# Performance work log

Hardware: AMD Instinct MI355X
Metric: run time of the kernel (lower is better)

The kernel has to match this reference:

```python
import jax, jax.numpy as jnp
import numpy as np

B, NK = 32, 1024
NUM_SAMPLES = 512
IT_MATCHES = 4
IT_RANSAC = 8
NUM_CORR = 5
INLIER_3D_TH = 0.15
INLIER_REF_TH = 0.15
NUM_REF_STEPS = 4
SCORE_TEMP = 10.0
TH_OUTLIERS = 0.35
MAX_LOSS_NULL = 0.5
SOFT_CLIP_M = 0.5
BETA = 5.0 / INLIER_3D_TH


def _gumbel(key, shape):
    u = jax.random.uniform(key, shape, minval=1e-6, maxval=1.0 - 1e-6)
    return -jnp.log(-jnp.log(u))


def _backproject(cor, d, K):
    # cor [B,S,2], d [B,S,2] (channel 0 is depth), K [B,3,3] -> [B,S,3]
    depth = d[..., :1]
    pts = jnp.concatenate([cor, jnp.ones_like(cor[..., :1])], -1)
    Kinv = jnp.linalg.inv(K)
    rays = jnp.einsum('bij,bsj->bsi', Kinv, pts)
    return depth * rays


def _procrustes(X, Y, w):
    # weighted Kabsch: find R,t with Y ~ R X + t. X,Y [B,N,3], w [B,N]
    wn = w / (jnp.sum(w, -1, keepdims=True) + 1e-8)
    muX = jnp.einsum('bn,bni->bi', wn, X)
    muY = jnp.einsum('bn,bni->bi', wn, Y)
    Xc = X - muX[:, None]
    Yc = Y - muY[:, None]
    H = jnp.einsum('bn,bni,bnj->bij', wn, Xc, Yc)  # [B,3,3]
    U, S, Vt = jnp.linalg.svd(H, full_matrices=False)
    V = jnp.swapaxes(Vt, -1, -2)
    Ut = jnp.swapaxes(U, -1, -2)
    d = jnp.linalg.det(V @ Ut)
    Vm = V * jnp.stack([jnp.ones_like(d), jnp.ones_like(d), d], -1)[:, None, :]
    R = Vm @ Ut
    t = muY - jnp.einsum('bij,bj->bi', R, muX)
    return R, t[:, None, :]


def _dist(X, Y, R, t):
    return jnp.linalg.norm(jnp.einsum('bij,bnj->bni', R, X) + t - Y, axis=-1)


def _pose_loss(R, t, Rgt, tgt):
    cosang = jnp.clip((jnp.einsum('bij,bij->b', R, Rgt) - 1.0) / 2.0, -0.999999, 0.999999)
    ang = jnp.arccos(cosang)
    terr = jnp.linalg.norm(t - tgt, axis=-1)[:, 0]
    sc = lambda x: SOFT_CLIP_M * jnp.tanh(x / SOFT_CLIP_M)
    lr = sc(ang)[:, None]
    lt = sc(terr)[:, None]
    return 0.5 * (lr + lt), lr, lt


def _rodrigues(axis, ang):
    x, y, z = axis[:, 0], axis[:, 1], axis[:, 2]
    zero = jnp.zeros_like(x)
    Kx = jnp.stack([zero, -z, y, z, zero, -x, -y, x, zero], -1).reshape(-1, 3, 3)
    I = jnp.eye(3, dtype=axis.dtype)[None]
    return I + jnp.sin(ang)[:, None, None] * Kx + (1.0 - jnp.cos(ang))[:, None, None] * (Kx @ Kx)


def setup_inputs():
    ks = jax.random.split(jax.random.key(0), 10)
    matches = jax.random.uniform(ks[0], (B, NK, NK), jnp.float32, 1e-4, 1.0)
    kps0 = jax.random.uniform(ks[1], (B, 2, NK), jnp.float32, 0.0, 640.0)
    kps1 = jax.random.uniform(ks[2], (B, 2, NK), jnp.float32, 0.0, 640.0)
    depth0 = jax.random.uniform(ks[3], (B, 2, NK), jnp.float32, 0.1, 10.0)
    depth1 = jax.random.uniform(ks[4], (B, 2, NK), jnp.float32, 0.1, 10.0)
    Kc = jnp.tile(jnp.array([[600.0, 0.0, 320.0], [0.0, 600.0, 240.0], [0.0, 0.0, 1.0]], jnp.float32)[None], (B, 1, 1))
    axis = jax.random.normal(ks[5], (B, 3))
    axis = axis / (jnp.linalg.norm(axis, axis=-1, keepdims=True) + 1e-8)
    ang = jax.random.uniform(ks[6], (B,), minval=0.0, maxval=0.5)
    R = _rodrigues(axis, ang)
    tvec = 0.3 * jax.random.normal(ks[7], (B, 3))
    T = jnp.zeros((B, 4, 4), jnp.float32).at[:, :3, :3].set(R).at[:, :3, 3].set(tvec).at[:, 3, 3].set(1.0)
    return dict(matches=matches, kps0=kps0, depth0=depth0, kps1=kps1, depth1=depth1,
                K0=Kc, K1=Kc, Kori_color0=Kc, T_0to1=T)


def _forward(matches, kps0, depth0, kps1, depth1, K0, K1, T_0to1):
    Rgt = T_0to1[:, :3, :3]
    tgt = T_0to1[:, :3, 3][:, None, :]
    matches_row = matches.reshape(B, NK * NK)
    logm = jnp.log(matches_row + 1e-12)
    bidx = jnp.arange(B)[:, None]
    kps0t = jnp.swapaxes(kps0, 1, 2)  # [B,NK,2]
    kps1t = jnp.swapaxes(kps1, 1, 2)
    d0t = jnp.swapaxes(depth0, 1, 2)
    d1t = jnp.swapaxes(depth1, 1, 2)
    key = jax.random.key(42)
    total = jnp.zeros((B, 1), jnp.float32)
    for _i in range(IT_MATCHES):
        key, km = jax.random.split(key)
        # multinomial-without-replacement via Gumbel top-k over the full match matrix
        _, sidx = jax.lax.top_k(logm + _gumbel(km, logm.shape), NUM_SAMPLES)  # [B,S]
        i0 = sidx // NK
        i1 = sidx % NK
        cor0 = kps0t[bidx, i0]
        cor1 = kps1t[bidx, i1]
        dd0 = d0t[bidx, i0]
        dd1 = d1t[bidx, i1]
        w = matches_row[bidx, sidx]  # sampling weights for RANSAC minimal sets
        X = _backproject(cor0, dd0, K0)
        Y = _backproject(cor1, dd1, K1)
        logw = jnp.log(w + 1e-12)
        scores, lvals = [], []
        for _kk in range(IT_RANSAC):
            key, kr = jax.random.split(key)
            _, ridx = jax.lax.top_k(logw + _gumbel(kr, logw.shape), NUM_CORR)  # [B,C]
            Xk = X[bidx, ridx]
            Yk = Y[bidx, ridx]
            R_pre, t_pre = _procrustes(Xk, Yk, jnp.ones((B, NUM_CORR), X.dtype))  # use_weights=False
            score_k = jnp.sum(jax.nn.sigmoid(BETA * (INLIER_3D_TH - _dist(X, Y, R_pre, t_pre))), -1, keepdims=True)
            # inlier refinement (no_grad in original)
            Xd = jax.lax.stop_gradient(X)
            Yd = jax.lax.stop_gradient(Y)
            Rd = jax.lax.stop_gradient(R_pre)
            td = jax.lax.stop_gradient(t_pre)
            inl_ref = jnp.zeros((B, NUM_SAMPLES), X.dtype).at[bidx, ridx].set(1.0)
            inl_pre = jnp.zeros((B,), X.dtype)
            for _r in range(NUM_REF_STEPS):
                inl = (_dist(Xd, Yd, Rd, td) < INLIER_REF_TH).astype(X.dtype)
                cnt = inl.sum(-1)
                do = (cnt >= NUM_CORR) & (cnt > inl_pre)
                inl_pre = cnt
                inl_ref = jnp.where(do[:, None], inl, inl_ref)
                Rn, tn = _procrustes(Xd, Yd, inl_ref)
                Rd = jnp.where(do[:, None, None], Rn, Rd)
                td = jnp.where(do[:, None, None], tn, td)
            R, t = _procrustes(X, Y, inl_ref)  # differentiable final fit
            lv, _lr, _lt = _pose_loss(R, t, Rgt, tgt)
            scores.append(score_k)
            lvals.append(lv)
        scores_r = jnp.concatenate(scores, -1)  # [B,IT_RANSAC]
        lvals_r = jnp.concatenate(lvals, -1)
        null_score = TH_OUTLIERS * NUM_SAMPLES * jnp.ones((B, 1), jnp.float32)
        null_loss = MAX_LOSS_NULL * jnp.ones((B, 1), jnp.float32)
        scores_n = jnp.concatenate([scores_r, null_score], -1)
        lvals_n = jnp.concatenate([lvals_r, null_loss], -1)
        sm = jax.nn.softmax(scores_n / SCORE_TEMP, -1)
        total = total + jnp.sum(lvals_n * sm, -1, keepdims=True)
    return total / IT_MATCHES


def reference(matches, kps0, depth0, kps1, depth1, K0, K1, Kori_color0, T_0to1):
    return _forward(matches, kps0, depth0, kps1, depth1, K0, K1, T_0to1)
```

## Files before the change

### kernel.cpp

```cpp
#include <hip/hip_runtime.h>
#include <stdint.h>

typedef unsigned long long u64;
typedef uint32_t u32;

#define NB 32
#define NKP 1024
#define ROWN (NKP*NKP)
#define NSAMP 512
#define ITM 4
#define ITR 8
#define NBIN 2048
#define KBASE 0xC0000000u
#define CHUNKS 64
#define SLOTS 256
#define WQ 352

struct Keys { u32 km[ITM][2]; u32 kr[ITM][ITR][2]; };

__host__ __device__ static inline u32 rotl32(u32 x, int d) { return __builtin_rotateleft32(x, (unsigned)d); }

__host__ __device__ static inline void tf2x32(u32 k0, u32 k1, u32 x0, u32 x1, u32& o0, u32& o1)
{
    u32 ks2 = k0 ^ k1 ^ 0x1BD11BDAu;
    x0 += k0; x1 += k1;
#define TFR(r) { x0 += x1; x1 = rotl32(x1, r); x1 ^= x0; }
    TFR(13) TFR(15) TFR(26) TFR(6)
    x0 += k1; x1 += ks2 + 1u;
    TFR(17) TFR(29) TFR(16) TFR(24)
    x0 += ks2; x1 += k0 + 2u;
    TFR(13) TFR(15) TFR(26) TFR(6)
    x0 += k0; x1 += k1 + 3u;
    TFR(17) TFR(29) TFR(16) TFR(24)
    x0 += k1; x1 += ks2 + 4u;
    TFR(13) TFR(15) TFR(26) TFR(6)
    x0 += ks2; x1 += k0 + 5u;
#undef TFR
    o0 = x0; o1 = x1;
}

__device__ static inline void tf4(const Keys& K, u32 flat, u32 bits[ITM])
{
    u32 x0[ITM], x1[ITM];
    #pragma unroll
    for (int i = 0; i < ITM; ++i) {
        x0[i] = K.km[i][0];
        x1[i] = flat + K.km[i][1];
    }
#define R4(rot) { _Pragma("unroll") \
    for (int i = 0; i < ITM; ++i) { x0[i] += x1[i]; x1[i] = rotl32(x1[i], rot); x1[i] ^= x0[i]; } }
#define INJ(a_expr, b_expr) { _Pragma("unroll") \
    for (int i = 0; i < ITM; ++i) { u32 k0 = K.km[i][0], k1 = K.km[i][1]; \
        u32 ks2 = k0 ^ k1 ^ 0x1BD11BDAu; (void)k0; (void)k1; (void)ks2; \
        x0[i] += (a_expr); x1[i] += (b_expr); } }
    R4(13) R4(15) R4(26) R4(6)
    INJ(k1,      ks2 + 1u)
    R4(17) R4(29) R4(16) R4(24)
    INJ(ks2,     k0 + 2u)
    R4(13) R4(15) R4(26) R4(6)
    INJ(k0,      k1 + 3u)
    R4(17) R4(29) R4(16) R4(24)
    INJ(k1,      ks2 + 4u)
    R4(13) R4(15) R4(26) R4(6)
    INJ(ks2,     k0 + 5u)
#undef R4
#undef INJ
    #pragma unroll
    for (int i = 0; i < ITM; ++i) bits[i] = x0[i] ^ x1[i];
}

#define G_MINV 1e-6f
#define G_MAXV ((float)(1.0 - 1e-6))
#define G_SPAN (G_MAXV - G_MINV)

__device__ static inline float u_from_bits(u32 bits) {
    float f = __uint_as_float((bits >> 9) | 0x3f800000u) - 1.0f;
    float u = __fadd_rn(__fmul_rn(f, G_SPAN), G_MINV);
    return fmaxf(G_MINV, u);
}

#define EARLY_TH9 (8220000u << 9)

__device__ static inline u32 fkey(float v) {
    u32 u = __float_as_uint(v);
    return (u & 0x80000000u) ? ~u : (u | 0x80000000u);
}

__device__ static inline float wred(float v) {
    #pragma unroll
    for (int o = 1; o < 64; o <<= 1) v += __shfl_xor(v, o, 64);
    return v;
}

__device__ static inline u64 shfl_xor_u64(u64 v, int mask) {
    u32 lo = (u32)v, hi = (u32)(v >> 32);
    lo = __shfl_xor(lo, mask, 64);
    hi = __shfl_xor(hi, mask, 64);
    return ((u64)hi << 32) | (u64)lo;
}

__device__ static void kabsch(const float Hf[9], float Rf[9])
{
    double H00=Hf[0],H01=Hf[1],H02=Hf[2];
    double H10=Hf[3],H11=Hf[4],H12=Hf[5];
    double H20=Hf[6],H21=Hf[7],H22=Hf[8];
    double A00 = H00*H00 + H10*H10 + H20*H20;
    double A01 = H00*H01 + H10*H11 + H20*H21;
    double A02 = H00*H02 + H10*H12 + H20*H22;
    double A11 = H01*H01 + H11*H11 + H21*H21;
    double A12 = H01*H02 + H11*H12 + H21*H22;
    double A22 = H02*H02 + H12*H12 + H22*H22;
    double V00=1,V10=0,V20=0;
    double V01=0,V11=1,V21=0;
    double V02=0,V12=0,V22=1;
#define JROT(App,Aqq,Apq,Apr,Aqr, Vp0,Vp1,Vp2, Vq0,Vq1,Vq2) \
    if (fabs(Apq) > 0.0) { \
        double th = (Aqq - App) / (2.0 * Apq); \
        double tt = copysign(1.0, th) / (fabs(th) + sqrt(1.0 + th*th)); \
        double cc = 1.0 / sqrt(1.0 + tt*tt); \
        double ss = tt * cc; \
        double npp = App - tt*Apq, nqq = Aqq + tt*Apq; \
        double npr = cc*Apr - ss*Aqr, nqr = ss*Apr + cc*Aqr; \
        App = npp; Aqq = nqq; Apq = 0.0; Apr = npr; Aqr = nqr; \
        double tv; \
        tv = cc*Vp0 - ss*Vq0; Vq0 = ss*Vp0 + cc*Vq0; Vp0 = tv; \
        tv = cc*Vp1 - ss*Vq1; Vq1 = ss*Vp1 + cc*Vq1; Vp1 = tv; \
        tv = cc*Vp2 - ss*Vq2; Vq2 = ss*Vp2 + cc*Vq2; Vp2 = tv; \
    }
    for (int sw = 0; sw < 5; ++sw) {
        JROT(A00,A11,A01, A02,A12, V00,V10,V20, V01,V11,V21);
        JROT(A00,A22,A02, A01,A12, V00,V10,V20, V02,V12,V22);
        JROT(A11,A22,A12, A01,A02, V01,V11,V21, V02,V12,V22);
    }
#undef JROT
    double l0=A00, l1=A11, l2=A22;
    double e0[3]={V00,V10,V20}, e1[3]={V01,V11,V21}, e2[3]={V02,V12,V22};
    if (l0 < l1) { double t=l0;l0=l1;l1=t; for(int c=0;c<3;++c){double s=e0[c];e0[c]=e1[c];e1[c]=s;} }
    if (l0 < l2) { double t=l0;l0=l2;l2=t; for(int c=0;c<3;++c){double s=e0[c];e0[c]=e2[c];e2[c]=s;} }
    if (l1 < l2) { double t=l1;l1=l2;l2=t; for(int c=0;c<3;++c){double s=e1[c];e1[c]=e2[c];e2[c]=s;} }
    double u0[3], u1[3], u2[3];
#define HMUL(e,u) { u[0]=H00*e[0]+H01*e[1]+H02*e[2]; u[1]=H10*e[0]+H11*e[1]+H12*e[2]; u[2]=H20*e[0]+H21*e[1]+H22*e[2]; }
    HMUL(e0,u0) HMUL(e1,u1) HMUL(e2,u2)
#undef HMUL
    double s0 = sqrt(u0[0]*u0[0]+u0[1]*u0[1]+u0[2]*u0[2]);
    double s1 = sqrt(u1[0]*u1[0]+u1[1]*u1[1]+u1[2]*u1[2]);
    double s2 = sqrt(u2[0]*u2[0]+u2[1]*u2[1]+u2[2]*u2[2]);
    double eps = 1e-12 + 1e-6 * s0;
    if (s0 > 0.0) { u0[0]/=s0; u0[1]/=s0; u0[2]/=s0; } else { u0[0]=1.0; u0[1]=0.0; u0[2]=0.0; }
    if (s1 > eps) { u1[0]/=s1; u1[1]/=s1; u1[2]/=s1; }
    else {
        double ax0 = (fabs(u0[0]) < 0.9) ? 1.0 : 0.0;
        double ax1 = 1.0 - ax0;
        double dd = ax0*u0[0] + ax1*u0[1];
        double w0 = ax0 - dd*u0[0], w1 = ax1 - dd*u0[1], w2 = -dd*u0[2];
        double nn = sqrt(w0*w0+w1*w1+w2*w2);
        u1[0]=w0/nn; u1[1]=w1/nn; u1[2]=w2/nn;
    }
    if (s2 > eps) { u2[0]/=s2; u2[1]/=s2; u2[2]/=s2; }
    else {
        u2[0] = u0[1]*u1[2] - u0[2]*u1[1];
        u2[1] = u0[2]*u1[0] - u0[0]*u1[2];
        u2[2] = u0[0]*u1[1] - u0[1]*u1[0];
    }
    double M[3][3];
    #pragma unroll
    for (int i2=0;i2<3;++i2)
      #pragma unroll
      for (int j2=0;j2<3;++j2)
        M[i2][j2] = e0[i2]*u0[j2] + e1[i2]*u1[j2] + e2[i2]*u2[j2];
    double det = M[0][0]*(M[1][1]*M[2][2]-M[1][2]*M[2][1])
               - M[0][1]*(M[1][0]*M[2][2]-M[1][2]*M[2][0])
               + M[0][2]*(M[1][0]*M[2][1]-M[1][1]*M[2][0]);
    #pragma unroll
    for (int i2=0;i2<3;++i2)
      #pragma unroll
      for (int j2=0;j2<3;++j2)
        Rf[i2*3+j2] = (float)(e0[i2]*u0[j2] + e1[i2]*u1[j2] + det*(e2[i2]*u2[j2]));
}

__device__ static inline float dist1(const float R[9], const float t[3], const float x[3], const float y[3])
{
    float a = R[0]*x[0]+R[1]*x[1]+R[2]*x[2]+t[0]-y[0];
    float b = R[3]*x[0]+R[4]*x[1]+R[5]*x[2]+t[1]-y[1];
    float c = R[6]*x[0]+R[7]*x[1]+R[8]*x[2]+t[2]-y[2];
    return sqrtf(a*a+b*b+c*c);
}

__device__ static void proc512(const float (&X)[8][3], const float (&Y)[8][3], const float (&w)[8],
                               float R[9], float t[3])
{
    float sw = 0.f;
    #pragma unroll
    for (int q=0;q<8;++q) sw += w[q];
    float S = wred(sw) + 1e-8f;
    float wn[8];
    #pragma unroll
    for (int q=0;q<8;++q) wn[q] = w[q] / S;
    float mx[3], my[3];
    #pragma unroll
    for (int c=0;c<3;++c) {
        float ax=0.f, ay=0.f;
        #pragma unroll
        for (int q=0;q<8;++q) { ax += wn[q]*X[q][c]; ay += wn[q]*Y[q][c]; }
        mx[c] = wred(ax); my[c] = wred(ay);
    }
    float Hf[9];
    #pragma unroll
    for (int ci=0;ci<3;++ci)
      #pragma unroll
      for (int cj=0;cj<3;++cj) {
        float h=0.f;
        #pragma unroll
        for (int q=0;q<8;++q) h += wn[q]*(X[q][ci]-mx[ci])*(Y[q][cj]-my[cj]);
        Hf[ci*3+cj] = wred(h);
      }
    kabsch(Hf, R);
    #pragma unroll
    for (int c=0;c<3;++c) t[c] = my[c] - (R[c*3+0]*mx[0] + R[c*3+1]*mx[1] + R[c*3+2]*mx[2]);
}

__device__ static void inv3(const float* __restrict__ Kin, float* __restrict__ out)
{
    float a[3][6];
    for (int r=0;r<3;++r) for (int c=0;c<3;++c) { a[r][c]=Kin[r*3+c]; a[r][c+3] = (r==c)?1.f:0.f; }
    for (int col=0; col<3; ++col) {
        int piv = col;
        for (int r=col+1;r<3;++r) if (fabsf(a[r][col]) > fabsf(a[piv][col])) piv = r;
        if (piv != col) for (int c=0;c<6;++c) { float tt=a[col][c]; a[col][c]=a[piv][c]; a[piv][c]=tt; }
        float pv = a[col][col];
        for (int c=0;c<6;++c) a[col][c] /= pv;
        for (int r=0;r<3;++r) if (r != col) {
            float f = a[r][col];
            if (f != 0.f) for (int c=0;c<6;++c) a[r][c] -= f * a[col][c];
        }
    }
    for (int r=0;r<3;++r) for (int c=0;c<3;++c) out[r*3+c] = a[r][c+3];
}

static const size_t OFF_CNTS = 0;
static const size_t OFF_SC   = OFF_CNTS + (size_t)ITM*NB*CHUNKS*4;
static const size_t OFF_LV   = OFF_SC   + (size_t)ITM*NB*ITR*4;
static const size_t OFF_SAMP = OFF_LV   + (size_t)ITM*NB*ITR*4;
static const size_t OFF_CAND = OFF_SAMP + (size_t)ITM*NB*NSAMP*8*4;

__device__ static inline void drain1(u64 e, float m, u64 (*lists)[SLOTS], u32* lcnt)
{
    u32 bits = (u32)(e >> 32);
    u32 i2 = ((u32)e >> 20) & 3u;
    u32 jj = (u32)e & 0xFFFFFu;
    float u = u_from_bits(bits);
    float g = -logf(-logf(u));
    float v = logf(m + 1e-12f) + g;
    if (v > 4.0f) {
        u32 p = atomicAdd(&lcnt[i2], 1u);
        if (p < (u32)SLOTS) lists[i2][p] = ((u64)fkey(v) << 32) | (u64)(u32)(~jj);
    }
}

__global__ __launch_bounds__(256) void kA(const float* __restrict__ mat, Keys keys,
                                          u64* __restrict__ candC, u32* __restrict__ cnts)
{
    __shared__ u64 lists[ITM][SLOTS];
    __shared__ u32 lcnt[ITM];
    __shared__ u64 q[4][WQ];
    int tid = threadIdx.x;
    int lane = tid & 63;
    int wid = tid >> 6;
    u64 lmask_lt = (1ull << lane) - 1ull;
    if (tid < ITM) lcnt[tid] = 0;
    __syncthreads();
    int b = blockIdx.y;
    int chunk = blockIdx.x;
    const float* rowb = mat + (size_t)b * ROWN;
    u32 jbase = (u32)chunk * 16384u + (u32)tid;
    for (int seg = 0; seg < 2; ++seg) {
        u32 cnt = 0;
        #pragma unroll 1
        for (int lp = 0; lp < 32; ++lp) {
            u32 j = jbase + (u32)((seg*32 + lp) << 8);
            u32 flat = ((u32)b << 20) | j;
            u32 bits[ITM];
            tf4(keys, flat, bits);
            #pragma unroll
            for (int i = 0; i < ITM; ++i) {
                bool hit = (bits[i] >= EARLY_TH9);
                u64 mask = __ballot(hit);
                if (hit) {
                    u32 pos = cnt + (u32)__popcll(mask & lmask_lt);
                    if (pos < (u32)WQ)
                        q[wid][pos] = ((u64)bits[i] << 32) | ((u64)(u32)i << 20) | (u64)j;
                }
                cnt += (u32)__popcll(mask);
            }
        }
        u32 qn = (cnt > (u32)WQ) ? (u32)WQ : cnt;
        for (u32 t0 = (u32)lane; t0 < qn; t0 += 256) {
            u32 t1 = t0 + 64, t2 = t0 + 128, t3 = t0 + 192;
            u64 e0 = q[wid][t0];
            float m0 = rowb[(u32)e0 & 0xFFFFFu];
            u64 e1 = 0, e2 = 0, e3 = 0;
            float m1 = 0.f, m2 = 0.f, m3 = 0.f;
            if (t1 < qn) { e1 = q[wid][t1]; m1 = rowb[(u32)e1 & 0xFFFFFu]; }
            if (t2 < qn) { e2 = q[wid][t2]; m2 = rowb[(u32)e2 & 0xFFFFFu]; }
            if (t3 < qn) { e3 = q[wid][t3]; m3 = rowb[(u32)e3 & 0xFFFFFu]; }
            drain1(e0, m0, lists, lcnt);
            if (t1 < qn) drain1(e1, m1, lists, lcnt);
            if (t2 < qn) drain1(e2, m2, lists, lcnt);
            if (t3 < qn) drain1(e3, m3, lists, lcnt);
        }
    }
    __syncthreads();
    #pragma unroll
    for (int i = 0; i < ITM; ++i) {
        u32 n = lcnt[i]; if (n > (u32)SLOTS) n = SLOTS;
        for (u32 s = tid; s < n; s += 256)
            candC[(((size_t)(i*NB + b))*CHUNKS + chunk)*SLOTS + s] = lists[i][s];
    }
    if (tid < ITM) cnts[((size_t)(tid*NB + b))*CHUNKS + chunk] = min(lcnt[tid], (u32)SLOTS);
}

__global__ __launch_bounds__(512) void kDE(const float* __restrict__ mat,
        const float* __restrict__ kps0, const float* __restrict__ dep0,
        const float* __restrict__ kps1, const float* __restrict__ dep1,
        const float* __restrict__ K0, const float* __restrict__ K1,
        const float* __restrict__ Tmat, Keys keys,
        const u64* __restrict__ candC, const u32* __restrict__ cnts,
        float* __restrict__ scoreArr, float* __restrict__ lvArr)
{
    int ib = blockIdx.x;
    int b = ib % NB;
    int i = ib / NB;
    int tid = threadIdx.x;
    int lane = tid & 63;
    int wid = tid >> 6;
    __shared__ u32 hist[NBIN];
    __shared__ u64 buf[1024];
    __shared__ float sampL[NSAMP][9];
    __shared__ u32 ccnt[CHUNKS];
    __shared__ u32 gs[64];
    __shared__ u32 nkeep, cutkey_s;
    __shared__ float Ki[2][9];
    for (int idx = tid; idx < NBIN; idx += 512) hist[idx] = 0;
    for (int idx = tid; idx < 1024; idx += 512) buf[idx] = 0ull;
    if (tid < CHUNKS) ccnt[tid] = cnts[(size_t)ib*CHUNKS + tid];
    if (tid == 0) nkeep = 0;
    __syncthreads();
    const u64* cd = candC + (size_t)ib * CHUNKS * SLOTS;
    for (int t = tid; t < CHUNKS*SLOTS; t += 512) {
        int c = t >> 8, s = t & (SLOTS-1);
        if ((u32)s < ccnt[c]) {
            u32 key = (u32)(cd[t] >> 32);
            u32 bin = (key - KBASE) >> 14;
            if (bin > (u32)(NBIN-1)) bin = NBIN-1;
            atomicAdd(&hist[bin], 1u);
        }
    }
    __syncthreads();
    if (tid < 64) {
        u32 ssum = 0;
        int top = NBIN-1 - tid*32;
        for (int k = 0; k < 32; ++k) ssum += hist[top - k];
        gs[tid] = ssum;
    }
    __syncthreads();
    if (tid == 0) {
        u32 cum = 0; int cutbin = -1;
        for (int g = 0; g < 64; ++g) {
            if (cum + gs[g] >= (u32)NSAMP) {
                int t2 = NBIN-1 - g*32;
                for (int k = 0; k < 32; ++k) {
                    u32 c = hist[t2 - k];
                    if (cum + c >= (u32)NSAMP) { cutbin = t2 - k; break; }
                    cum += c;
                }
                break;
            }
            cum += gs[g];
        }
        cutkey_s = (cutbin >= 0) ? (KBASE + ((u32)cutbin << 14)) : 0u;
    }
    __syncthreads();
    u32 cutkey = cutkey_s;
    for (int t = tid; t < CHUNKS*SLOTS; t += 512) {
        int c = t >> 8, s = t & (SLOTS-1);
        if ((u32)s < ccnt[c]) {
            u64 cv = cd[t];
            if ((u32)(cv >> 32) >= cutkey) {
                u32 p = atomicAdd(&nkeep, 1u);
                if (p < 1024u) buf[p] = cv;
            }
        }
    }
    __syncthreads();
    for (int k = 2; k <= 1024; k <<= 1) {
        for (int j = k >> 1; j > 0; j >>= 1) {
            for (int i2 = tid; i2 < 1024; i2 += 512) {
                int ixj = i2 ^ j;
                if (ixj > i2) {
                    bool up = ((i2 & k) == 0);
                    u64 a = buf[i2], c2 = buf[ixj];
                    bool dosw = up ? (a > c2) : (a < c2);
                    if (dosw) { buf[i2] = c2; buf[ixj] = a; }
                }
            }
            __syncthreads();
        }
    }
    if (tid == 0) { inv3(K0 + (size_t)b*9, Ki[0]); inv3(K1 + (size_t)b*9, Ki[1]); }
    __syncthreads();
    {
        int r = tid;
        if (r < NSAMP) {
            u64 c = buf[1023 - r];
            u32 j = (~(u32)(c & 0xFFFFFFFFull)) & (u32)(ROWN - 1);
            int i0 = (int)(j >> 10);
            int i1 = (int)(j & 1023u);
            float uu0 = kps0[(size_t)b*2*NKP + i0];
            float vv0 = kps0[(size_t)b*2*NKP + NKP + i0];
            float dd0 = dep0[(size_t)b*2*NKP + i0];
            float uu1 = kps1[(size_t)b*2*NKP + i1];
            float vv1 = kps1[(size_t)b*2*NKP + NKP + i1];
            float dd1 = dep1[(size_t)b*2*NKP + i1];
            float r0 = Ki[0][0]*uu0 + Ki[0][1]*vv0 + Ki[0][2];
            float r1 = Ki[0][3]*uu0 + Ki[0][4]*vv0 + Ki[0][5];
            float r2 = Ki[0][6]*uu0 + Ki[0][7]*vv0 + Ki[0][8];
            float q0 = Ki[1][0]*uu1 + Ki[1][1]*vv1 + Ki[1][2];
            float q1 = Ki[1][3]*uu1 + Ki[1][4]*vv1 + Ki[1][5];
            float q2 = Ki[1][6]*uu1 + Ki[1][7]*vv1 + Ki[1][8];
            float w = mat[(size_t)b*ROWN + j];
            sampL[r][0] = dd0*r0; sampL[r][1] = dd0*r1; sampL[r][2] = dd0*r2;
            sampL[r][3] = dd1*q0; sampL[r][4] = dd1*q1; sampL[r][5] = dd1*q2;
            sampL[r][6] = logf(w + 1e-12f);
        }
    }
    __syncthreads();
    int kk = wid;
    float X[8][3], Y[8][3], lw[8];
    #pragma unroll
    for (int q2 = 0; q2 < 8; ++q2) {
        const float* sp = &sampL[q2*64 + lane][0];
        X[q2][0]=sp[0]; X[q2][1]=sp[1]; X[q2][2]=sp[2];
        Y[q2][0]=sp[3]; Y[q2][1]=sp[4]; Y[q2][2]=sp[5];
        lw[q2]=sp[6];
    }
    u64 comp[8];
    #pragma unroll
    for (int q2 = 0; q2 < 8; ++q2) {
        u32 j = (u32)(q2*64 + lane);
        u32 o0,o1; tf2x32(keys.kr[i][kk][0], keys.kr[i][kk][1], 0u, (u32)(b*NSAMP) + j, o0,o1);
        float u = u_from_bits(o0^o1);
        float g = -logf(-logf(u));
        float v = lw[q2] + g;
        comp[q2] = ((u64)fkey(v) << 32) | (u64)(u32)(~j);
    }
    int ridx[5];
    #pragma unroll
    for (int r = 0; r < 5; ++r) {
        u64 m = comp[0];
        #pragma unroll
        for (int q2=1;q2<8;++q2) if (comp[q2] > m) m = comp[q2];
        #pragma unroll
        for (int o=1;o<64;o<<=1) { u64 x = shfl_xor_u64(m,o); if (x > m) m = x; }
        ridx[r] = (int)((~(u32)(m & 0xFFFFFFFFull)) & (u32)(NSAMP-1));
        #pragma unroll
        for (int q2=0;q2<8;++q2) if (comp[q2] == m) comp[q2] = 0ull;
    }
    float Xk[5][3], Yk[5][3];
    #pragma unroll
    for (int r=0;r<5;++r) {
        const float* p = &sampL[ridx[r]][0];
        Xk[r][0]=p[0]; Xk[r][1]=p[1]; Xk[r][2]=p[2];
        Yk[r][0]=p[3]; Yk[r][1]=p[4]; Yk[r][2]=p[5];
    }
    float S5 = 5.0f + 1e-8f;
    float wn5 = 1.0f / S5;
    float mx[3]={0,0,0}, my[3]={0,0,0};
    #pragma unroll
    for (int r=0;r<5;++r) {
        #pragma unroll
        for (int c=0;c<3;++c) { mx[c] += wn5*Xk[r][c]; my[c] += wn5*Yk[r][c]; }
    }
    float Hf[9] = {0,0,0,0,0,0,0,0,0};
    #pragma unroll
    for (int r=0;r<5;++r)
      #pragma unroll
      for (int ci=0;ci<3;++ci)
        #pragma unroll
        for (int cj=0;cj<3;++cj)
          Hf[ci*3+cj] += wn5*(Xk[r][ci]-mx[ci])*(Yk[r][cj]-my[cj]);
    float Rpre[9], tpre[3];
    kabsch(Hf, Rpre);
    #pragma unroll
    for (int c=0;c<3;++c) tpre[c] = my[c] - (Rpre[c*3+0]*mx[0] + Rpre[c*3+1]*mx[1] + Rpre[c*3+2]*mx[2]);
    const float BETAF = (float)(5.0/0.15);
    float partial = 0.f;
    #pragma unroll
    for (int q2=0;q2<8;++q2) {
        float d = dist1(Rpre, tpre, X[q2], Y[q2]);
        float z = BETAF * (0.15f - d);
        partial += 1.0f / (1.0f + expf(-z));
    }
    float score = wred(partial);
    float inlref[8];
    #pragma unroll
    for (int q2=0;q2<8;++q2) {
        int j = q2*64 + lane;
        inlref[q2] = (j==ridx[0] || j==ridx[1] || j==ridx[2] || j==ridx[3] || j==ridx[4]) ? 1.0f : 0.0f;
    }
    float Rd[9], td[3];
    #pragma unroll
    for (int c2=0;c2<9;++c2) Rd[c2]=Rpre[c2];
    td[0]=tpre[0]; td[1]=tpre[1]; td[2]=tpre[2];
    float inl_pre = 0.f;
    for (int step=0; step<4; ++step) {
        float inl[8]; float csum = 0.f;
        #pragma unroll
        for (int q2=0;q2<8;++q2) {
            float d = dist1(Rd, td, X[q2], Y[q2]);
            inl[q2] = (d < 0.15f) ? 1.0f : 0.0f;
            csum += inl[q2];
        }
        float cnt = wred(csum);
        bool doit = (cnt >= 5.0f) && (cnt > inl_pre);
        inl_pre = cnt;
        if (doit) {
            #pragma unroll
            for (int q2=0;q2<8;++q2) inlref[q2] = inl[q2];
            proc512(X, Y, inlref, Rd, td);
        }
    }
    float Rfin[9], tfin[3];
    proc512(X, Y, inlref, Rfin, tfin);
    const float* Tb = Tmat + (size_t)b*16;
    float tr = 0.f;
    #pragma unroll
    for (int ci=0;ci<3;++ci)
      #pragma unroll
      for (int cj=0;cj<3;++cj)
        tr += Rfin[ci*3+cj] * Tb[ci*4+cj];
    float cosang = (tr - 1.0f) * 0.5f;
    cosang = fminf(fmaxf(cosang, -0.999999f), 0.999999f);
    float ang = acosf(cosang);
    float d0 = tfin[0]-Tb[3], d1 = tfin[1]-Tb[7], d2 = tfin[2]-Tb[11];
    float terr = sqrtf(d0*d0 + d1*d1 + d2*d2);
    float lr = 0.5f * tanhf(ang / 0.5f);
    float lt = 0.5f * tanhf(terr / 0.5f);
    float lv = 0.5f * (lr + lt);
    if (lane == 0) { scoreArr[ib*ITR + kk] = score; lvArr[ib*ITR + kk] = lv; }
}

__global__ void kF(const float* __restrict__ scoreArr, const float* __restrict__ lvArr, float* __restrict__ out)
{
    int b = threadIdx.x;
    if (b >= NB) return;
    const float NULLSC = (float)(0.35 * 512.0);
    float total = 0.f;
    for (int i = 0; i < ITM; ++i) {
        float x[9], lvv[9], ee[9];
        for (int k = 0; k < 8; ++k) {
            x[k] = scoreArr[(i*NB + b)*ITR + k] / 10.0f;
            lvv[k] = lvArr[(i*NB + b)*ITR + k];
        }
        x[8] = NULLSC / 10.0f;
        lvv[8] = 0.5f;
        float m = x[0];
        for (int k = 1; k < 9; ++k) m = fmaxf(m, x[k]);
        float Ssum = 0.f;
        for (int k = 0; k < 9; ++k) { ee[k] = expf(x[k] - m); Ssum += ee[k]; }
        float acc = 0.f;
        for (int k = 0; k < 9; ++k) acc += lvv[k] * (ee[k] / Ssum);
        total += acc;
    }
    out[b] = total / 4.0f;
}

extern "C" void kernel_launch(void* const* d_in, const int* in_sizes, int n_in,
                              void* d_out, int out_size, void* d_ws, size_t ws_size,
                              hipStream_t stream)
{
    (void)in_sizes; (void)n_in; (void)out_size; (void)ws_size;
    const float* mat  = (const float*)d_in[0];
    const float* kps0 = (const float*)d_in[1];
    const float* dep0 = (const float*)d_in[2];
    const float* kps1 = (const float*)d_in[3];
    const float* dep1 = (const float*)d_in[4];
    const float* K0   = (const float*)d_in[5];
    const float* K1   = (const float*)d_in[6];
    const float* Tm   = (const float*)d_in[8];
    float* out = (float*)d_out;

    Keys keys;
    {
        u32 k0 = 0u, k1 = 42u;
        for (int i = 0; i < ITM; ++i) {
            u32 a0,a1,b0,b1;
            tf2x32(k0,k1, 0u,0u, a0,a1);
            tf2x32(k0,k1, 0u,1u, b0,b1);
            k0=a0; k1=a1; keys.km[i][0]=b0; keys.km[i][1]=b1;
            for (int kk = 0; kk < ITR; ++kk) {
                tf2x32(k0,k1, 0u,0u, a0,a1);
                tf2x32(k0,k1, 0u,1u, b0,b1);
                k0=a0; k1=a1; keys.kr[i][kk][0]=b0; keys.kr[i][kk][1]=b1;
            }
        }
    }
    char* ws = (char*)d_ws;
    u32* cnts       = (u32*)(ws + OFF_CNTS);
    float* scoreArr = (float*)(ws + OFF_SC);
    float* lvArr    = (float*)(ws + OFF_LV);
    u64* candC      = (u64*)(ws + OFF_CAND);

    kA<<<dim3(CHUNKS, NB), 256, 0, stream>>>(mat, keys, candC, cnts);
    kDE<<<ITM*NB, 512, 0, stream>>>(mat, kps0, dep0, kps1, dep1, K0, K1, Tm, keys,
                                    candC, cnts, scoreArr, lvArr);
    kF<<<1, 64, 0, stream>>>(scoreArr, lvArr, out);
}
```

Measured before the change: 337.2 us.

## Move match gather and Gumbel scoring from kA into kDE candidate scan

kA now only runs the threefry filter and writes raw per-wave hit records to global memory. It no longer gathers match values, computes Gumbel scores or compacts into per-iteration shared lists. kDE reads all four iterations' records for its batch, filters by its iteration index, and recomputes the match gather and log-Gumbel score in both the histogram pass and the selection pass. This shrinks kA and removes its shared-memory drain phase. In exchange each kDE block scans a much larger candidate buffer that holds records from all iterations, and it repeats the gather and log math twice.

Result: slower. 706.6 us (+109.5%).

```diff
diff --git a/kernel.cpp b/kernel.cpp
--- a/kernel.cpp
+++ b/kernel.cpp
@@ -13,8 +13,7 @@
 #define NBIN 2048
 #define KBASE 0xC0000000u
 #define CHUNKS 64
-#define SLOTS 256
-#define WQ 352
+#define WCAP 512
 
 struct Keys { u32 km[ITM][2]; u32 kr[ITM][ITR][2]; };
 
@@ -237,86 +236,41 @@
     for (int r=0;r<3;++r) for (int c=0;c<3;++c) out[r*3+c] = a[r][c+3];
 }
 
-static const size_t OFF_CNTS = 0;
-static const size_t OFF_SC   = OFF_CNTS + (size_t)ITM*NB*CHUNKS*4;
+static const size_t OFF_CNT2 = 0;
+static const size_t OFF_SC   = OFF_CNT2 + (size_t)NB*CHUNKS*4*4;
 static const size_t OFF_LV   = OFF_SC   + (size_t)ITM*NB*ITR*4;
-static const size_t OFF_SAMP = OFF_LV   + (size_t)ITM*NB*ITR*4;
-static const size_t OFF_CAND = OFF_SAMP + (size_t)ITM*NB*NSAMP*8*4;
-
-__device__ static inline void drain1(u64 e, float m, u64 (*lists)[SLOTS], u32* lcnt)
-{
-    u32 bits = (u32)(e >> 32);
-    u32 i2 = ((u32)e >> 20) & 3u;
-    u32 jj = (u32)e & 0xFFFFFu;
-    float u = u_from_bits(bits);
-    float g = -logf(-logf(u));
-    float v = logf(m + 1e-12f) + g;
-    if (v > 4.0f) {
-        u32 p = atomicAdd(&lcnt[i2], 1u);
-        if (p < (u32)SLOTS) lists[i2][p] = ((u64)fkey(v) << 32) | (u64)(u32)(~jj);
-    }
-}
-
-__global__ __launch_bounds__(256) void kA(const float* __restrict__ mat, Keys keys,
-                                          u64* __restrict__ candC, u32* __restrict__ cnts)
-{
-    __shared__ u64 lists[ITM][SLOTS];
-    __shared__ u32 lcnt[ITM];
-    __shared__ u64 q[4][WQ];
+static const size_t OFF_CANDW= OFF_LV   + (size_t)ITM*NB*ITR*4 + 64;
+
+__global__ __launch_bounds__(256) void kA(Keys keys, u64* __restrict__ candW, u32* __restrict__ cnts2)
+{
     int tid = threadIdx.x;
     int lane = tid & 63;
     int wid = tid >> 6;
     u64 lmask_lt = (1ull << lane) - 1ull;
-    if (tid < ITM) lcnt[tid] = 0;
-    __syncthreads();
     int b = blockIdx.y;
     int chunk = blockIdx.x;
-    const float* rowb = mat + (size_t)b * ROWN;
+    u64* wq = candW + ((size_t)((b*CHUNKS + chunk)*4 + wid)) * WCAP;
+    u32 cnt = 0;
     u32 jbase = (u32)chunk * 16384u + (u32)tid;
-    for (int seg = 0; seg < 2; ++seg) {
-        u32 cnt = 0;
-        #pragma unroll 1
-        for (int lp = 0; lp < 32; ++lp) {
-            u32 j = jbase + (u32)((seg*32 + lp) << 8);
-            u32 flat = ((u32)b << 20) | j;
-            u32 bits[ITM];
-            tf4(keys, flat, bits);
-            #pragma unroll
-            for (int i = 0; i < ITM; ++i) {
-                bool hit = (bits[i] >= EARLY_TH9);
-                u64 mask = __ballot(hit);
-                if (hit) {
-                    u32 pos = cnt + (u32)__popcll(mask & lmask_lt);
-                    if (pos < (u32)WQ)
-                        q[wid][pos] = ((u64)bits[i] << 32) | ((u64)(u32)i << 20) | (u64)j;
-                }
-                cnt += (u32)__popcll(mask);
+    #pragma unroll 1
+    for (int lp = 0; lp < 64; ++lp) {
+        u32 j = jbase + ((u32)lp << 8);
+        u32 flat = ((u32)b << 20) | j;
+        u32 bits[ITM];
+        tf4(keys, flat, bits);
+        #pragma unroll
+        for (int i = 0; i < ITM; ++i) {
+            bool hit = (bits[i] >= EARLY_TH9);
+            u64 mask = __ballot(hit);
+            if (hit) {
+                u32 pos = cnt + (u32)__popcll(mask & lmask_lt);
+                if (pos < (u32)WCAP)
+                    wq[pos] = ((u64)bits[i] << 32) | (u64)(((u32)i << 20) | j);
             }
-        }
-        u32 qn = (cnt > (u32)WQ) ? (u32)WQ : cnt;
-        for (u32 t0 = (u32)lane; t0 < qn; t0 += 256) {
-            u32 t1 = t0 + 64, t2 = t0 + 128, t3 = t0 + 192;
-            u64 e0 = q[wid][t0];
-            float m0 = rowb[(u32)e0 & 0xFFFFFu];
-            u64 e1 = 0, e2 = 0, e3 = 0;
-            float m1 = 0.f, m2 = 0.f, m3 = 0.f;
-            if (t1 < qn) { e1 = q[wid][t1]; m1 = rowb[(u32)e1 & 0xFFFFFu]; }
-            if (t2 < qn) { e2 = q[wid][t2]; m2 = rowb[(u32)e2 & 0xFFFFFu]; }
-            if (t3 < qn) { e3 = q[wid][t3]; m3 = rowb[(u32)e3 & 0xFFFFFu]; }
-            drain1(e0, m0, lists, lcnt);
-            if (t1 < qn) drain1(e1, m1, lists, lcnt);
-            if (t2 < qn) drain1(e2, m2, lists, lcnt);
-            if (t3 < qn) drain1(e3, m3, lists, lcnt);
-        }
-    }
-    __syncthreads();
-    #pragma unroll
-    for (int i = 0; i < ITM; ++i) {
-        u32 n = lcnt[i]; if (n > (u32)SLOTS) n = SLOTS;
-        for (u32 s = tid; s < n; s += 256)
-            candC[(((size_t)(i*NB + b))*CHUNKS + chunk)*SLOTS + s] = lists[i][s];
-    }
-    if (tid < ITM) cnts[((size_t)(tid*NB + b))*CHUNKS + chunk] = min(lcnt[tid], (u32)SLOTS);
+            cnt += (u32)__popcll(mask);
+        }
+    }
+    if (lane == 0) cnts2[(size_t)((b*CHUNKS + chunk)*4 + wid)] = min(cnt, (u32)WCAP);
 }
 
 __global__ __launch_bounds__(512) void kDE(const float* __restrict__ mat,
@@ -324,7 +278,7 @@
         const float* __restrict__ kps1, const float* __restrict__ dep1,
         const float* __restrict__ K0, const float* __restrict__ K1,
         const float* __restrict__ Tmat, Keys keys,
-        const u64* __restrict__ candC, const u32* __restrict__ cnts,
+        const u64* __restrict__ candW, const u32* __restrict__ cnts2,
         float* __restrict__ scoreArr, float* __restrict__ lvArr)
 {
     int ib = blockIdx.x;
@@ -336,23 +290,36 @@
     __shared__ u32 hist[NBIN];
     __shared__ u64 buf[1024];
     __shared__ float sampL[NSAMP][9];
-    __shared__ u32 ccnt[CHUNKS];
+    __shared__ u32 cw[CHUNKS*4];
     __shared__ u32 gs[64];
     __shared__ u32 nkeep, cutkey_s;
     __shared__ float Ki[2][9];
     for (int idx = tid; idx < NBIN; idx += 512) hist[idx] = 0;
     for (int idx = tid; idx < 1024; idx += 512) buf[idx] = 0ull;
-    if (tid < CHUNKS) ccnt[tid] = cnts[(size_t)ib*CHUNKS + tid];
+    for (int idx = tid; idx < CHUNKS*4; idx += 512) cw[idx] = cnts2[(size_t)b*CHUNKS*4 + idx];
     if (tid == 0) nkeep = 0;
     __syncthreads();
-    const u64* cd = candC + (size_t)ib * CHUNKS * SLOTS;
-    for (int t = tid; t < CHUNKS*SLOTS; t += 512) {
-        int c = t >> 8, s = t & (SLOTS-1);
-        if ((u32)s < ccnt[c]) {
-            u32 key = (u32)(cd[t] >> 32);
-            u32 bin = (key - KBASE) >> 14;
-            if (bin > (u32)(NBIN-1)) bin = NBIN-1;
-            atomicAdd(&hist[bin], 1u);
+    const u64* cb = candW + (size_t)b*CHUNKS*4*WCAP;
+    const float* rowb = mat + (size_t)b * ROWN;
+    for (int t = tid; t < CHUNKS*4*WCAP; t += 512) {
+        int slot = t & (WCAP-1);
+        int cwv = t >> 9;
+        if ((u32)slot < cw[cwv]) {
+            u64 rec = cb[t];
+            u32 lo = (u32)rec;
+            if (((lo >> 20) & 3u) == (u32)i) {
+                u32 jj = lo & 0xFFFFFu;
+                float m = rowb[jj];
+                float u = u_from_bits((u32)(rec >> 32));
+                float g = -logf(-logf(u));
+                float v = logf(m + 1e-12f) + g;
+                if (v > 4.0f) {
+                    u32 key = fkey(v);
+                    u32 bin = (key - KBASE) >> 14;
+                    if (bin > (u32)(NBIN-1)) bin = NBIN-1;
+                    atomicAdd(&hist[bin], 1u);
+                }
+            }
         }
     }
     __syncthreads();
@@ -381,13 +348,25 @@
     }
     __syncthreads();
     u32 cutkey = cutkey_s;
-    for (int t = tid; t < CHUNKS*SLOTS; t += 512) {
-        int c = t >> 8, s = t & (SLOTS-1);
-        if ((u32)s < ccnt[c]) {
-            u64 cv = cd[t];
-            if ((u32)(cv >> 32) >= cutkey) {
-                u32 p = atomicAdd(&nkeep, 1u);
-                if (p < 1024u) buf[p] = cv;
+    for (int t = tid; t < CHUNKS*4*WCAP; t += 512) {
+        int slot = t & (WCAP-1);
+        int cwv = t >> 9;
+        if ((u32)slot < cw[cwv]) {
+            u64 rec = cb[t];
+            u32 lo = (u32)rec;
+            if (((lo >> 20) & 3u) == (u32)i) {
+                u32 jj = lo & 0xFFFFFu;
+                float m = rowb[jj];
+                float u = u_from_bits((u32)(rec >> 32));
+                float g = -logf(-logf(u));
+                float v = logf(m + 1e-12f) + g;
+                if (v > 4.0f) {
+                    u32 key = fkey(v);
+                    if (key >= cutkey) {
+                        u32 p = atomicAdd(&nkeep, 1u);
+                        if (p < 1024u) buf[p] = ((u64)key << 32) | (u64)(u32)(~jj);
+                    }
+                }
             }
         }
     }
@@ -605,13 +584,13 @@
         }
     }
     char* ws = (char*)d_ws;
-    u32* cnts       = (u32*)(ws + OFF_CNTS);
+    u32* cnts2      = (u32*)(ws + OFF_CNT2);
     float* scoreArr = (float*)(ws + OFF_SC);
     float* lvArr    = (float*)(ws + OFF_LV);
-    u64* candC      = (u64*)(ws + OFF_CAND);
-
-    kA<<<dim3(CHUNKS, NB), 256, 0, stream>>>(mat, keys, candC, cnts);
+    u64* candW      = (u64*)(ws + OFF_CANDW);
+
+    kA<<<dim3(CHUNKS, NB), 256, 0, stream>>>(keys, candW, cnts2);
     kDE<<<ITM*NB, 512, 0, stream>>>(mat, kps0, dep0, kps1, dep1, K0, K1, Tm, keys,
-                                    candC, cnts, scoreArr, lvArr);
+                                    candW, cnts2, scoreArr, lvArr);
     kF<<<1, 64, 0, stream>>>(scoreArr, lvArr, out);
 }
```
